# Kernel tuning notes

Hardware: AMD Instinct MI355X
Metric: run time of the kernel (lower is better)

Reference implementation:

```python
import jax, jax.numpy as jnp
import numpy as np
from jax import lax


def _causal_mask(shape, mask_center):
    # shape = (out_ch, in_ch, h, w); mirrors CausalConv2d mask construction
    o, i, h, w = shape
    m = np.zeros(shape, dtype=np.float32)
    m[:, :, : h // 2, :] = 1.0
    m[:, :, h // 2, : w // 2 + (0 if mask_center else 1)] = 1.0
    return jnp.asarray(m)

MASK1 = _causal_mask((16, 1, 7, 7), mask_center=True)
MASK2 = _causal_mask((16, 16, 3, 3), mask_center=False)


def _conv(x, w, b, pad):
    y = lax.conv_general_dilated(
        x, w, window_strides=(1, 1), padding=[(pad, pad), (pad, pad)],
        dimension_numbers=("NCHW", "OIHW", "NCHW"))
    return y + b[None, :, None, None]


def setup_inputs() -> dict:
    key = jax.random.key(0)
    ks = jax.random.split(key, 7)
    B, H, W = 1024, 64, 64
    x = jax.random.uniform(ks[0], (B, 1, H, W), dtype=jnp.float32)
    # Kaiming-ish init scales
    w1 = jax.random.normal(ks[1], (16, 1, 7, 7), jnp.float32) * (1.0 / np.sqrt(1 * 49))
    b1 = jax.random.normal(ks[2], (16,), jnp.float32) * 0.01
    w2 = jax.random.normal(ks[3], (16, 16, 3, 3), jnp.float32) * (1.0 / np.sqrt(16 * 9))
    b2 = jax.random.normal(ks[4], (16,), jnp.float32) * 0.01
    w3 = jax.random.normal(ks[5], (1, 16, 1, 1), jnp.float32) * (1.0 / np.sqrt(16))
    b3 = jax.random.normal(ks[6], (1,), jnp.float32) * 0.01
    return {"x": x, "w1": w1, "b1": b1, "w2": w2, "b2": b2, "w3": w3, "b3": b3}


def reference(x, w1, b1, w2, b2, w3, b3):
    # PixelCNN._forward: masked conv7x7 -> relu -> masked conv3x3 -> relu -> conv1x1 -> sigmoid
    h = jax.nn.relu(_conv(x, w1 * MASK1, b1, pad=3))
    h = jax.nn.relu(_conv(h, w2 * MASK2, b2, pad=1))
    return jax.nn.sigmoid(_conv(h, w3, b3, pad=0))
```

## Files before the change

### kernel.cpp

```cpp
#include <hip/hip_runtime.h>

typedef _Float16 half8  __attribute__((ext_vector_type(8)));
typedef __fp16   fp16x2 __attribute__((ext_vector_type(2)));
typedef float    floatx4 __attribute__((ext_vector_type(4)));
typedef float    f4a __attribute__((ext_vector_type(4), aligned(4)));

#define IMG_H 64
#define IMG_W 64
#define TH 8
#define INH 12
#define INW 72
#define H1W 66
#define H1H 9
#define PLDW (H1H*H1W*2)
#define CP 880
#define CPM1 879
#define S16N (4*CP + 4)

__device__ __forceinline__ unsigned pk2u(float a, float b) {
    fp16x2 h = __builtin_amdgcn_cvt_pkrtz(a, b);
    return __builtin_bit_cast(unsigned, h);
}

__global__ __launch_bounds__(256, 8) void pixelcnn_mfma17(
    const float* __restrict__ x,
    const float* __restrict__ w1, const float* __restrict__ b1,
    const float* __restrict__ w2, const float* __restrict__ b2,
    const float* __restrict__ w3, const float* __restrict__ b3,
    float* __restrict__ out)
{
    __shared__ __align__(16) _Float16      s16[S16N];
    __shared__ __align__(16) unsigned char s_w2t8[16 * 96];
    __shared__ __align__(16) unsigned      s_h1[2 * PLDW];

    const int t    = threadIdx.x;
    const int lane = t & 63;
    const int wave = t >> 6;
    const int n    = lane & 15;
    const int quad = lane >> 4;
    const int img  = blockIdx.y;
    const int ty0  = blockIdx.x * TH;

    const float* xim = x + img * (IMG_H * IMG_W);

    const float* wr = w1 + n * 49 + quad * 7;
    f4a wlo = *(const f4a*)wr;
    f4a whi = *(const f4a*)(wr + 3);
    const floatx4 bias1 = *(const floatx4*)(b1 + quad * 4);
    const floatx4 bias2 = *(const floatx4*)(b2 + quad * 4);
    const floatx4 w3q   = *(const floatx4*)(w3 + quad * 4);
    const float   bias3 = b3[0];
    half8 af;
    {
        bool q3 = (quad == 3);
        af[0] = (_Float16)wlo[0];
        af[1] = (_Float16)wlo[1];
        af[2] = (_Float16)wlo[2];
        af[3] = (_Float16)(q3 ? 0.f : wlo[3]);
        af[4] = (_Float16)(q3 ? 0.f : whi[1]);
        af[5] = (_Float16)(q3 ? 0.f : whi[2]);
        af[6] = (_Float16)(q3 ? 0.f : whi[3]);
        af[7] = (_Float16)0.f;
    }

    if (t < 216) {
        int r = t / 18, c4 = (t - r * 18) * 4;
        int gy = ty0 - 4 + r;
        int gx0 = c4 - 4;
        float4 v  = {0.f, 0.f, 0.f, 0.f};
        float4 v2 = {0.f, 0.f, 0.f, 0.f};
        if ((unsigned)gy < IMG_H) {
            const float* rp = xim + gy * IMG_W;
            if ((unsigned)gx0 < IMG_W)       v  = *(const float4*)(rp + gx0);
            if ((unsigned)(gx0 + 4) < IMG_W) v2 = *(const float4*)(rp + gx0 + 4);
        }
        unsigned a0 = pk2u(v.x,  v.y),  a1 = pk2u(v.z,  v.w);
        unsigned a2 = pk2u(v2.x, v2.y), a3 = pk2u(v2.z, v2.w);
        unsigned m10 = __builtin_amdgcn_alignbit(a1, a0, 16);
        unsigned m21 = __builtin_amdgcn_alignbit(a2, a1, 16);
        unsigned m32 = __builtin_amdgcn_alignbit(a3, a2, 16);
        int lin = r * INW + c4;
        *(uint2*)&s16[0*CP + 4 + lin] = uint2{a0,  a1 };
        *(uint2*)&s16[1*CP + 4 + lin] = uint2{m10, m21};
        *(uint2*)&s16[2*CP + 4 + lin] = uint2{a1,  a2 };
        *(uint2*)&s16[3*CP + 4 + lin] = uint2{m21, m32};
    } else if (t < 234) {
        int idx = t - 216;
        int cell = (idx >> 1) * H1W + ((idx & 1) ? 65 : 0);
        *(uint2*)&s_h1[cell * 2]        = uint2{0u, 0u};
        *(uint2*)&s_h1[PLDW + cell * 2] = uint2{0u, 0u};
    }
    if (t < 128) {
        int ch = t >> 3, l2 = t & 7;
        const float* r0 = w2 + (ch * 16 + 2 * l2) * 9;
        const float* r1 = r0 + 9;
#pragma unroll
        for (int j = 0; j < 6; ++j) {
            float v0 = (j < 5) ? r0[j] : 0.f;
            float v1 = (j < 5) ? r1[j] : 0.f;
            unsigned q8 = (unsigned)__builtin_amdgcn_cvt_pk_fp8_f32(v0, v1, 0, false);
            *(unsigned short*)&s_w2t8[ch * 96 + j * 16 + 2 * l2] = (unsigned short)(q8 & 0xffff);
        }
    }
    __syncthreads();

    {
        const int px = wave * 16 + n;
        const int S  = px + 1;
        const int c  = S & 3;
        const _Float16* ap0 = &s16[c * CPM1 + 4 + S + quad * INW];
        const unsigned wd0 = (unsigned)((quad >> 1) * PLDW + S * 2 + (quad & 1));
        const bool top = (ty0 == 0);

#pragma unroll
        for (int i = 0; i < H1H; ++i) {
            const _Float16* ap = ap0 + i * INW;
            uint2 lo = *(const uint2*)ap;
            uint2 hi = *(const uint2*)(ap + 4);
            uint4 bu; bu.x = lo.x; bu.y = lo.y; bu.z = hi.x; bu.w = hi.y;
            half8 b = __builtin_bit_cast(half8, bu);
            floatx4 acc = bias1;
            acc = __builtin_amdgcn_mfma_f32_16x16x32_f16(af, b, acc, 0, 0, 0);
            int d = __builtin_amdgcn_cvt_pk_fp8_f32(fmaxf(acc[0], 0.f), fmaxf(acc[1], 0.f), 0, false);
            d = __builtin_amdgcn_cvt_pk_fp8_f32(fmaxf(acc[2], 0.f), fmaxf(acc[3], 0.f), d, true);
            unsigned dv = (unsigned)d;
            if (i == 0 && top) dv = 0u;
            s_h1[wd0 + i * (H1W * 2)] = dv;
        }
    }
    __syncthreads();

    {
        const long w2f0 = *(const long*)&s_w2t8[n * 96 +  0 + quad * 8];
        const long w2f1 = *(const long*)&s_w2t8[n * 96 + 32 + quad * 8];
        const long w2f2 = *(const long*)&s_w2t8[n * 96 + 64 + quad * 8];
        const int x0 = wave * 16;
        const int tqh = quad >> 1, plane = quad & 1;
        const int E0 = H1W + x0 + n + 1;
        const char* h1b = (const char*)s_h1 + plane * (PLDW * 4);
        const char* a0 = h1b + (E0 - H1W - 1 + tqh) * 8;
        const char* a1 = h1b + (E0 + (tqh ? -1 : -(H1W - 1))) * 8;
        const char* a2 = h1b + E0 * 8;
        float* sbase = out + ((img * IMG_H) + ty0 + quad) * IMG_W + x0 + n;

#pragma unroll
        for (int g = 0; g < 2; ++g) {
            float sv0, sv1, sv2, sv3;
#pragma unroll
            for (int q = 0; q < 4; ++q) {
                const int k = g * 4 + q;
                floatx4 acc = bias2;
                acc = __builtin_amdgcn_mfma_f32_16x16x32_fp8_fp8(w2f0, *(const long*)(a0 + k * 528), acc, 0, 0, 0);
                acc = __builtin_amdgcn_mfma_f32_16x16x32_fp8_fp8(w2f1, *(const long*)(a1 + k * 528), acc, 0, 0, 0);
                acc = __builtin_amdgcn_mfma_f32_16x16x32_fp8_fp8(w2f2, *(const long*)(a2 + k * 528), acc, 0, 0, 0);
                float sacc = fmaxf(acc[0], 0.f) * w3q[0];
                sacc = fmaf(fmaxf(acc[1], 0.f), w3q[1], sacc);
                sacc = fmaf(fmaxf(acc[2], 0.f), w3q[2], sacc);
                sacc = fmaf(fmaxf(acc[3], 0.f), w3q[3], sacc);
                sacc += __shfl_xor(sacc, 16);
                sacc += __shfl_xor(sacc, 32);
                if      (q == 0) sv0 = sacc;
                else if (q == 1) sv1 = sacc;
                else if (q == 2) sv2 = sacc;
                else             sv3 = sacc;
            }
            float t01 = (quad & 1) ? sv1 : sv0;
            float t23 = (quad & 1) ? sv3 : sv2;
            float v   = (quad & 2) ? t23 : t01;
            float r = __builtin_amdgcn_rcpf(1.f + __expf(-(v + bias3)));
            *(float*)((char*)sbase + g * 1024) = r;
        }
    }
}

extern "C" void kernel_launch(void* const* d_in, const int* in_sizes, int n_in,
                              void* d_out, int out_size, void* d_ws, size_t ws_size,
                              hipStream_t stream) {
    const float* x  = (const float*)d_in[0];
    const float* w1 = (const float*)d_in[1];
    const float* b1 = (const float*)d_in[2];
    const float* w2 = (const float*)d_in[3];
    const float* b2 = (const float*)d_in[4];
    const float* w3 = (const float*)d_in[5];
    const float* b3 = (const float*)d_in[6];
    float* out = (float*)d_out;

    dim3 grid(8, 1024);
    dim3 block(256);
    hipLaunchKernelGGL(pixelcnn_mfma17, grid, block, 0, stream,
                       x, w1, b1, w2, b2, w3, b3, out);
}
```

Measured before the change: 102.6 us.

## Recompute h1 halo columns per wave to drop the inter-stage block barrier

```diff
diff --git a/kernel.cpp b/kernel.cpp
--- a/kernel.cpp
+++ b/kernel.cpp
@@ -8,7 +8,6 @@
 #define IMG_H 64
 #define IMG_W 64
 #define TH 8
-#define INH 12
 #define INW 72
 #define H1W 66
 #define H1H 9
@@ -22,7 +21,13 @@
     return __builtin_bit_cast(unsigned, h);
 }
 
-__global__ __launch_bounds__(256, 8) void pixelcnn_mfma17(
+__device__ __forceinline__ unsigned relu_pk8(floatx4 acc) {
+    int d = __builtin_amdgcn_cvt_pk_fp8_f32(fmaxf(acc[0], 0.f), fmaxf(acc[1], 0.f), 0, false);
+    d = __builtin_amdgcn_cvt_pk_fp8_f32(fmaxf(acc[2], 0.f), fmaxf(acc[3], 0.f), d, true);
+    return (unsigned)d;
+}
+
+__global__ __launch_bounds__(256, 8) void pixelcnn_mfma18(
     const float* __restrict__ x,
     const float* __restrict__ w1, const float* __restrict__ b1,
     const float* __restrict__ w2, const float* __restrict__ b2,
@@ -84,11 +89,6 @@
         *(uint2*)&s16[1*CP + 4 + lin] = uint2{m10, m21};
         *(uint2*)&s16[2*CP + 4 + lin] = uint2{a1,  a2 };
         *(uint2*)&s16[3*CP + 4 + lin] = uint2{m21, m32};
-    } else if (t < 234) {
-        int idx = t - 216;
-        int cell = (idx >> 1) * H1W + ((idx & 1) ? 65 : 0);
-        *(uint2*)&s_h1[cell * 2]        = uint2{0u, 0u};
-        *(uint2*)&s_h1[PLDW + cell * 2] = uint2{0u, 0u};
     }
     if (t < 128) {
         int ch = t >> 3, l2 = t & 7;
@@ -104,8 +104,9 @@
     }
     __syncthreads();
 
+    const int x0 = wave * 16;
     {
-        const int px = wave * 16 + n;
+        const int px = x0 + n;
         const int S  = px + 1;
         const int c  = S & 3;
         const _Float16* ap0 = &s16[c * CPM1 + 4 + S + quad * INW];
@@ -121,20 +122,45 @@
             half8 b = __builtin_bit_cast(half8, bu);
             floatx4 acc = bias1;
             acc = __builtin_amdgcn_mfma_f32_16x16x32_f16(af, b, acc, 0, 0, 0);
-            int d = __builtin_amdgcn_cvt_pk_fp8_f32(fmaxf(acc[0], 0.f), fmaxf(acc[1], 0.f), 0, false);
-            d = __builtin_amdgcn_cvt_pk_fp8_f32(fmaxf(acc[2], 0.f), fmaxf(acc[3], 0.f), d, true);
-            unsigned dv = (unsigned)d;
+            unsigned dv = relu_pk8(acc);
             if (i == 0 && top) dv = 0u;
             s_h1[wd0 + i * (H1W * 2)] = dv;
         }
-    }
-    __syncthreads();
+
+        const int Lb   = n >> 3;
+        const int hcol = x0 + Lb * 17;
+        const bool obm = Lb ? (wave == 3) : (wave == 0);
+        const int ebase = 4 + x0 + Lb * 896;
+        const unsigned wdh = (unsigned)((quad >> 1) * PLDW + hcol * 2 + (quad & 1));
+        {
+            const int rn = (n & 7) + 1;
+            const _Float16* aph = &s16[ebase + (rn + quad) * INW];
+            uint2 lo = *(const uint2*)aph;
+            uint2 hi = *(const uint2*)(aph + 4);
+            uint4 bu; bu.x = lo.x; bu.y = lo.y; bu.z = hi.x; bu.w = hi.y;
+            half8 b = __builtin_bit_cast(half8, bu);
+            floatx4 acc = bias1;
+            acc = __builtin_amdgcn_mfma_f32_16x16x32_f16(af, b, acc, 0, 0, 0);
+            unsigned dv = obm ? 0u : relu_pk8(acc);
+            s_h1[wdh + rn * (H1W * 2)] = dv;
+        }
+        {
+            const _Float16* aph = &s16[ebase + quad * INW];
+            uint2 lo = *(const uint2*)aph;
+            uint2 hi = *(const uint2*)(aph + 4);
+            uint4 bu; bu.x = lo.x; bu.y = lo.y; bu.z = hi.x; bu.w = hi.y;
+            half8 b = __builtin_bit_cast(half8, bu);
+            floatx4 acc = bias1;
+            acc = __builtin_amdgcn_mfma_f32_16x16x32_f16(af, b, acc, 0, 0, 0);
+            unsigned dv = (obm || top) ? 0u : relu_pk8(acc);
+            s_h1[wdh] = dv;
+        }
+    }
 
     {
         const long w2f0 = *(const long*)&s_w2t8[n * 96 +  0 + quad * 8];
         const long w2f1 = *(const long*)&s_w2t8[n * 96 + 32 + quad * 8];
         const long w2f2 = *(const long*)&s_w2t8[n * 96 + 64 + quad * 8];
-        const int x0 = wave * 16;
         const int tqh = quad >> 1, plane = quad & 1;
         const int E0 = H1W + x0 + n + 1;
         const char* h1b = (const char*)s_h1 + plane * (PLDW * 4);
@@ -187,6 +213,6 @@
 
     dim3 grid(8, 1024);
     dim3 block(256);
-    hipLaunchKernelGGL(pixelcnn_mfma17, grid, block, 0, stream,
+    hipLaunchKernelGGL(pixelcnn_mfma18, grid, block, 0, stream,
                        x, w1, b1, w2, b2, w3, b3, out);
 }
```

Result: no change. 103.9 us (+1.3%).

## Switch masked 3x3 conv to 32x32x16 fp8 MFMA with tap-wise weight layout

Applied to the files above, without the earlier changes.

```diff
diff --git a/kernel.cpp b/kernel.cpp
--- a/kernel.cpp
+++ b/kernel.cpp
@@ -3,12 +3,12 @@
 typedef _Float16 half8  __attribute__((ext_vector_type(8)));
 typedef __fp16   fp16x2 __attribute__((ext_vector_type(2)));
 typedef float    floatx4 __attribute__((ext_vector_type(4)));
+typedef float    f32x16 __attribute__((ext_vector_type(16)));
 typedef float    f4a __attribute__((ext_vector_type(4), aligned(4)));
 
 #define IMG_H 64
 #define IMG_W 64
 #define TH 8
-#define INH 12
 #define INW 72
 #define H1W 66
 #define H1H 9
@@ -22,7 +22,7 @@
     return __builtin_bit_cast(unsigned, h);
 }
 
-__global__ __launch_bounds__(256, 8) void pixelcnn_mfma17(
+__global__ __launch_bounds__(256, 4) void pixelcnn_mfma19(
     const float* __restrict__ x,
     const float* __restrict__ w1, const float* __restrict__ b1,
     const float* __restrict__ w2, const float* __restrict__ b2,
@@ -30,7 +30,7 @@
     float* __restrict__ out)
 {
     __shared__ __align__(16) _Float16      s16[S16N];
-    __shared__ __align__(16) unsigned char s_w2t8[16 * 96];
+    __shared__ __align__(16) unsigned char s_w2A[32 * 80];
     __shared__ __align__(16) unsigned      s_h1[2 * PLDW];
 
     const int t    = threadIdx.x;
@@ -38,6 +38,8 @@
     const int wave = t >> 6;
     const int n    = lane & 15;
     const int quad = lane >> 4;
+    const int l31  = lane & 31;
+    const int hi   = lane >> 5;
     const int img  = blockIdx.y;
     const int ty0  = blockIdx.x * TH;
 
@@ -47,8 +49,10 @@
     f4a wlo = *(const f4a*)wr;
     f4a whi = *(const f4a*)(wr + 3);
     const floatx4 bias1 = *(const floatx4*)(b1 + quad * 4);
-    const floatx4 bias2 = *(const floatx4*)(b2 + quad * 4);
-    const floatx4 w3q   = *(const floatx4*)(w3 + quad * 4);
+    const floatx4 b2q0 = *(const floatx4*)(b2 + 0),  b2q1 = *(const floatx4*)(b2 + 4);
+    const floatx4 b2q2 = *(const floatx4*)(b2 + 8),  b2q3 = *(const floatx4*)(b2 + 12);
+    const floatx4 w3q0 = *(const floatx4*)(w3 + 0),  w3q1 = *(const floatx4*)(w3 + 4);
+    const floatx4 w3q2 = *(const floatx4*)(w3 + 8),  w3q3 = *(const floatx4*)(w3 + 12);
     const float   bias3 = b3[0];
     half8 af;
     {
@@ -90,17 +94,24 @@
         *(uint2*)&s_h1[cell * 2]        = uint2{0u, 0u};
         *(uint2*)&s_h1[PLDW + cell * 2] = uint2{0u, 0u};
     }
-    if (t < 128) {
-        int ch = t >> 3, l2 = t & 7;
-        const float* r0 = w2 + (ch * 16 + 2 * l2) * 9;
-        const float* r1 = r0 + 9;
-#pragma unroll
-        for (int j = 0; j < 6; ++j) {
-            float v0 = (j < 5) ? r0[j] : 0.f;
-            float v1 = (j < 5) ? r1[j] : 0.f;
-            unsigned q8 = (unsigned)__builtin_amdgcn_cvt_pk_fp8_f32(v0, v1, 0, false);
-            *(unsigned short*)&s_w2t8[ch * 96 + j * 16 + 2 * l2] = (unsigned short)(q8 & 0xffff);
-        }
+    if (t < 160) {
+        int row = (t * 205) >> 10;
+        int tap = t - row * 5;
+        uint4 w4 = {0u, 0u, 0u, 0u};
+        if (!(row & 4)) {
+            int o = (row & 3) | ((row & 24) >> 1);
+            const float* wp = w2 + (o * 16) * 9 + tap;
+            unsigned d0 = (unsigned)__builtin_amdgcn_cvt_pk_fp8_f32(wp[0],   wp[9],   0,  false);
+            d0          = (unsigned)__builtin_amdgcn_cvt_pk_fp8_f32(wp[18],  wp[27],  d0, true);
+            unsigned d1 = (unsigned)__builtin_amdgcn_cvt_pk_fp8_f32(wp[36],  wp[45],  0,  false);
+            d1          = (unsigned)__builtin_amdgcn_cvt_pk_fp8_f32(wp[54],  wp[63],  d1, true);
+            unsigned d2 = (unsigned)__builtin_amdgcn_cvt_pk_fp8_f32(wp[72],  wp[81],  0,  false);
+            d2          = (unsigned)__builtin_amdgcn_cvt_pk_fp8_f32(wp[90],  wp[99],  d2, true);
+            unsigned d3 = (unsigned)__builtin_amdgcn_cvt_pk_fp8_f32(wp[108], wp[117], 0,  false);
+            d3          = (unsigned)__builtin_amdgcn_cvt_pk_fp8_f32(wp[126], wp[135], d3, true);
+            w4 = uint4{d0, d1, d2, d3};
+        }
+        *(uint4*)&s_w2A[row * 80 + tap * 16] = w4;
     }
     __syncthreads();
 
@@ -116,8 +127,8 @@
         for (int i = 0; i < H1H; ++i) {
             const _Float16* ap = ap0 + i * INW;
             uint2 lo = *(const uint2*)ap;
-            uint2 hi = *(const uint2*)(ap + 4);
-            uint4 bu; bu.x = lo.x; bu.y = lo.y; bu.z = hi.x; bu.w = hi.y;
+            uint2 hi2 = *(const uint2*)(ap + 4);
+            uint4 bu; bu.x = lo.x; bu.y = lo.y; bu.z = hi2.x; bu.w = hi2.y;
             half8 b = __builtin_bit_cast(half8, bu);
             floatx4 acc = bias1;
             acc = __builtin_amdgcn_mfma_f32_16x16x32_f16(af, b, acc, 0, 0, 0);
@@ -131,44 +142,49 @@
     __syncthreads();
 
     {
-        const long w2f0 = *(const long*)&s_w2t8[n * 96 +  0 + quad * 8];
-        const long w2f1 = *(const long*)&s_w2t8[n * 96 + 32 + quad * 8];
-        const long w2f2 = *(const long*)&s_w2t8[n * 96 + 64 + quad * 8];
-        const int x0 = wave * 16;
-        const int tqh = quad >> 1, plane = quad & 1;
-        const int E0 = H1W + x0 + n + 1;
-        const char* h1b = (const char*)s_h1 + plane * (PLDW * 4);
-        const char* a0 = h1b + (E0 - H1W - 1 + tqh) * 8;
-        const char* a1 = h1b + (E0 + (tqh ? -1 : -(H1W - 1))) * 8;
-        const char* a2 = h1b + E0 * 8;
-        float* sbase = out + ((img * IMG_H) + ty0 + quad) * IMG_W + x0 + n;
+        const char* wab = (const char*)s_w2A + l31 * 80 + hi * 8;
+        const long wA0 = *(const long*)(wab +  0);
+        const long wA1 = *(const long*)(wab + 16);
+        const long wA2 = *(const long*)(wab + 32);
+        const long wA3 = *(const long*)(wab + 48);
+        const long wA4 = *(const long*)(wab + 64);
+        const int colhalf = wave & 1, yhalf = wave >> 1;
+        const char* hb = (const char*)s_h1 + hi * (PLDW * 4);
+        const char* bb = hb + ((yhalf * 4) * H1W + colhalf * 32 + l31 + 1) * 8;
+        f32x16 biasC;
+        biasC[0]=b2q0[0]; biasC[1]=b2q0[1]; biasC[2]=b2q0[2]; biasC[3]=b2q0[3];
+        biasC[4]=b2q1[0]; biasC[5]=b2q1[1]; biasC[6]=b2q1[2]; biasC[7]=b2q1[3];
+        biasC[8]=b2q2[0]; biasC[9]=b2q2[1]; biasC[10]=b2q2[2]; biasC[11]=b2q2[3];
+        biasC[12]=b2q3[0]; biasC[13]=b2q3[1]; biasC[14]=b2q3[2]; biasC[15]=b2q3[3];
+        float* sbase = out + ((img * IMG_H) + ty0 + yhalf * 4) * IMG_W + colhalf * 32 + l31;
 
 #pragma unroll
-        for (int g = 0; g < 2; ++g) {
-            float sv0, sv1, sv2, sv3;
-#pragma unroll
-            for (int q = 0; q < 4; ++q) {
-                const int k = g * 4 + q;
-                floatx4 acc = bias2;
-                acc = __builtin_amdgcn_mfma_f32_16x16x32_fp8_fp8(w2f0, *(const long*)(a0 + k * 528), acc, 0, 0, 0);
-                acc = __builtin_amdgcn_mfma_f32_16x16x32_fp8_fp8(w2f1, *(const long*)(a1 + k * 528), acc, 0, 0, 0);
-                acc = __builtin_amdgcn_mfma_f32_16x16x32_fp8_fp8(w2f2, *(const long*)(a2 + k * 528), acc, 0, 0, 0);
-                float sacc = fmaxf(acc[0], 0.f) * w3q[0];
-                sacc = fmaf(fmaxf(acc[1], 0.f), w3q[1], sacc);
-                sacc = fmaf(fmaxf(acc[2], 0.f), w3q[2], sacc);
-                sacc = fmaf(fmaxf(acc[3], 0.f), w3q[3], sacc);
-                sacc += __shfl_xor(sacc, 16);
-                sacc += __shfl_xor(sacc, 32);
-                if      (q == 0) sv0 = sacc;
-                else if (q == 1) sv1 = sacc;
-                else if (q == 2) sv2 = sacc;
-                else             sv3 = sacc;
-            }
-            float t01 = (quad & 1) ? sv1 : sv0;
-            float t23 = (quad & 1) ? sv3 : sv2;
-            float v   = (quad & 2) ? t23 : t01;
-            float r = __builtin_amdgcn_rcpf(1.f + __expf(-(v + bias3)));
-            *(float*)((char*)sbase + g * 1024) = r;
+        for (int j = 0; j < 4; ++j) {
+            f32x16 acc = biasC;
+            acc = __builtin_amdgcn_mfma_f32_32x32x16_fp8_fp8(wA0, *(const long*)(bb + (j * 66 - 1) * 8), acc, 0, 0, 0);
+            acc = __builtin_amdgcn_mfma_f32_32x32x16_fp8_fp8(wA1, *(const long*)(bb + (j * 66    ) * 8), acc, 0, 0, 0);
+            acc = __builtin_amdgcn_mfma_f32_32x32x16_fp8_fp8(wA2, *(const long*)(bb + (j * 66 + 1) * 8), acc, 0, 0, 0);
+            acc = __builtin_amdgcn_mfma_f32_32x32x16_fp8_fp8(wA3, *(const long*)(bb + ((j + 1) * 66 - 1) * 8), acc, 0, 0, 0);
+            acc = __builtin_amdgcn_mfma_f32_32x32x16_fp8_fp8(wA4, *(const long*)(bb + ((j + 1) * 66    ) * 8), acc, 0, 0, 0);
+            float s;
+            s = fmaxf(acc[0],  0.f) * w3q0[0];
+            s = fmaf(fmaxf(acc[1],  0.f), w3q0[1], s);
+            s = fmaf(fmaxf(acc[2],  0.f), w3q0[2], s);
+            s = fmaf(fmaxf(acc[3],  0.f), w3q0[3], s);
+            s = fmaf(fmaxf(acc[4],  0.f), w3q1[0], s);
+            s = fmaf(fmaxf(acc[5],  0.f), w3q1[1], s);
+            s = fmaf(fmaxf(acc[6],  0.f), w3q1[2], s);
+            s = fmaf(fmaxf(acc[7],  0.f), w3q1[3], s);
+            s = fmaf(fmaxf(acc[8],  0.f), w3q2[0], s);
+            s = fmaf(fmaxf(acc[9],  0.f), w3q2[1], s);
+            s = fmaf(fmaxf(acc[10], 0.f), w3q2[2], s);
+            s = fmaf(fmaxf(acc[11], 0.f), w3q2[3], s);
+            s = fmaf(fmaxf(acc[12], 0.f), w3q3[0], s);
+            s = fmaf(fmaxf(acc[13], 0.f), w3q3[1], s);
+            s = fmaf(fmaxf(acc[14], 0.f), w3q3[2], s);
+            s = fmaf(fmaxf(acc[15], 0.f), w3q3[3], s);
+            float r = __builtin_amdgcn_rcpf(1.f + __expf(-(s + bias3)));
+            if (lane < 32) *(float*)((char*)sbase + j * 256) = r;
         }
     }
 }
@@ -187,6 +203,6 @@
 
     dim3 grid(8, 1024);
     dim3 block(256);
-    hipLaunchKernelGGL(pixelcnn_mfma17, grid, block, 0, stream,
+    hipLaunchKernelGGL(pixelcnn_mfma19, grid, block, 0, stream,
                        x, w1, b1, w2, b2, w3, b3, out);
 }
```

Result: slower. 106.3 us (+3.7%).
